# Performance work log

Measured on AMD Instinct MI355X. Metric: run time of the kernel, lower is better.

## Reference

```python
import jax, jax.numpy as jnp
import numpy as np

B, N, C, H = 2, 2048, 1024, 16
D = C // H
SCALE = D ** -0.5


def setup_inputs() -> dict:
    key = jax.random.key(0)
    ks = jax.random.split(key, 5)
    x = jax.random.normal(ks[0], (B, N, C), dtype=jnp.float32)
    # causal mask, broadcast over batch: True = attend
    attention_mask = jnp.broadcast_to(jnp.tril(jnp.ones((N, N), dtype=bool)), (B, N, N))
    w_qkv = jax.random.normal(ks[1], (3 * C, C), dtype=jnp.float32) * (C ** -0.5)
    b_qkv = jax.random.normal(ks[2], (3 * C,), dtype=jnp.float32) * 0.02
    w_proj = jax.random.normal(ks[3], (C, C), dtype=jnp.float32) * (C ** -0.5)
    b_proj = jax.random.normal(ks[4], (C,), dtype=jnp.float32) * 0.02
    return {"x": x, "attention_mask": attention_mask, "w_qkv": w_qkv,
            "b_qkv": b_qkv, "w_proj": w_proj, "b_proj": b_proj}


def reference(x, attention_mask, w_qkv, b_qkv, w_proj, b_proj):
    b, n, c = x.shape
    qkv = x @ w_qkv.T + b_qkv                      # [B,N,3C]
    qkv = qkv.reshape(b, n, 3, H, D).transpose(2, 0, 3, 1, 4)  # [3,B,H,N,D]
    q, k, v = qkv[0], qkv[1], qkv[2]
    dots = jnp.einsum('bhid,bhjd->bhij', q, k) * SCALE
    mask_value = -jnp.finfo(dots.dtype).max
    dots = jnp.where(attention_mask[:, None, :, :], dots, mask_value)
    attn = jax.nn.softmax(dots.astype(jnp.float32), axis=-1).astype(dots.dtype)
    out = jnp.einsum('bhij,bhjd->bhid', attn, v)   # [B,H,N,D]
    # NOTE: original code reshapes WITHOUT transposing heads back - faithful.
    out = out.reshape(b, n, c)
    return out @ w_proj.T + b_proj
```

## Files before the change

kernel.cpp:

```cpp
#include <hip/hip_runtime.h>
#include <hip/hip_bf16.h>
#include <stdint.h>

#define SL_F 0.18033688011112043f

typedef unsigned short u16;
typedef unsigned int u32;
typedef __attribute__((ext_vector_type(8))) short bf16x8;
typedef __attribute__((ext_vector_type(4))) float f32x4;

__device__ __forceinline__ u16 f2bf(float f) {
    union { float f; u32 u; } v; v.f = f;
    return (u16)((v.u + 0x7fffu + ((v.u >> 16) & 1u)) >> 16);
}
__device__ __forceinline__ u32 pack2bf(float a, float b) {
    union { __hip_bfloat162 h; u32 u; } p;
    p.h = __float22bfloat162_rn(make_float2(a, b));
    return p.u;
}

__device__ __forceinline__ void gl_lds16(const u16* g, u16* l) {
    __builtin_amdgcn_global_load_lds(
        (const __attribute__((address_space(1))) u32*)g,
        (__attribute__((address_space(3))) u32*)l, 16, 0, 0);
}

__global__ __launch_bounds__(256) void convert_k(
    const float4* __restrict__ x, const float4* __restrict__ w1,
    const float4* __restrict__ w2,
    ushort4* __restrict__ xb, ushort4* __restrict__ w1b, ushort4* __restrict__ w2b)
{
    const int i = blockIdx.x * 256 + threadIdx.x;
    const int XN = 4096 * 1024 / 4, W1 = 3072 * 1024 / 4;
    float4 v; ushort4* dst;
    if (i < XN)            { v = x[i];            dst = &xb[i]; }
    else if (i < XN + W1)  { v = w1[i - XN];      dst = &w1b[i - XN]; }
    else                   { v = w2[i - XN - W1]; dst = &w2b[i - XN - W1]; }
    ushort4 o;
    o.x = f2bf(v.x); o.y = f2bf(v.y); o.z = f2bf(v.z); o.w = f2bf(v.w);
    *dst = o;
}

template<int NT, int EPI>
__global__ __launch_bounds__(256) void gemm_nt(
    const u16* __restrict__ A, const u16* __restrict__ Bw,
    const float* __restrict__ bias,
    u16* __restrict__ Qb, u16* __restrict__ Kb, u16* __restrict__ VTb,
    float* __restrict__ Out)
{
    constexpr int NBF = NT / 32;
    constexpr int BGRP = NT / 16;
    __shared__ __align__(16) u16 Al[2][8 * 512];
    __shared__ __align__(16) u16 Bl[2][BGRP * 512];
    const int tid = threadIdx.x;
    const int lane = tid & 63;
    const int w = tid >> 6;
    const int la = lane & 15, qd = lane >> 4;
    const int K = 1024;
    const int m0 = blockIdx.y * 128;
    const int n0 = blockIdx.x * NT;
    const int wm = (w >> 1) * 64, wn = (w & 1) * (NT / 2);

    const u16* Ag0 = A + (size_t)(m0 + (2 * w) * 16 + la) * K + qd * 8;
    const u16* Ag1 = A + (size_t)(m0 + (2 * w + 1) * 16 + la) * K + qd * 8;
    const int bg0 = (BGRP == 8) ? 2 * w : w;
    const u16* Bg0 = Bw + (size_t)(n0 + bg0 * 16 + la) * K + qd * 8;
    const u16* Bg1 = Bw + (size_t)(n0 + (2 * w + 1) * 16 + la) * K + qd * 8;

    auto stage = [&](int k0, int b) {
        gl_lds16(Ag0 + k0, &Al[b][(2 * w) * 512]);
        gl_lds16(Ag1 + k0, &Al[b][(2 * w + 1) * 512]);
        gl_lds16(Bg0 + k0, &Bl[b][bg0 * 512]);
        if (BGRP == 8)
            gl_lds16(Bg1 + k0, &Bl[b][(2 * w + 1) * 512]);
    };

    f32x4 acc[4][NBF] = {};
    int buf = 0;
    stage(0, 0);

    for (int k0 = 0; k0 < K; k0 += 32) {
        __syncthreads();
        if (k0 + 32 < K) stage(k0 + 32, buf ^ 1);

        bf16x8 af[4], bfr[NBF];
#pragma unroll
        for (int i = 0; i < 4; i++)
            af[i] = *(const bf16x8*)&Al[buf][(((unsigned)wm >> 4) + i) * 512 + lane * 8];
#pragma unroll
        for (int j = 0; j < NBF; j++)
            bfr[j] = *(const bf16x8*)&Bl[buf][(((unsigned)wn >> 4) + j) * 512 + lane * 8];
#pragma unroll
        for (int i = 0; i < 4; i++)
#pragma unroll
            for (int j = 0; j < NBF; j++)
                acc[i][j] = __builtin_amdgcn_mfma_f32_16x16x32_bf16(
                    af[i], bfr[j], acc[i][j], 0, 0, 0);
        buf ^= 1;
    }

#pragma unroll
    for (int j = 0; j < NBF; j++) {
        const int col = n0 + wn + j * 16 + la;
        const float bv = bias[col];
        if (EPI == 0) {
            const int t = col >> 10, hd = col & 1023, h = hd >> 6, d = hd & 63;
#pragma unroll
            for (int i = 0; i < 4; i++)
#pragma unroll
                for (int r = 0; r < 4; r++) {
                    const int row = m0 + wm + i * 16 + qd * 4 + r;
                    const int b = row >> 11, n = row & 2047;
                    const int bh = b * 16 + h;
                    const u16 val = f2bf(acc[i][j][r] + bv);
                    if (t == 0)      Qb[((size_t)bh * 2048 + n) * 64 + d] = val;
                    else if (t == 1) Kb[((size_t)bh * 2048 + n) * 64 + d] = val;
                    else             VTb[((size_t)bh * 64 + d) * 2048 + n] = val;
                }
        } else {
#pragma unroll
            for (int i = 0; i < 4; i++)
#pragma unroll
                for (int r = 0; r < 4; r++) {
                    const int row = m0 + wm + i * 16 + qd * 4 + r;
                    Out[(size_t)row * 1024 + col] = acc[i][j][r] + bv;
                }
        }
    }
}

__global__ __launch_bounds__(256) void attn_k(
    const u16* __restrict__ Qb, const u16* __restrict__ Kb,
    const u16* __restrict__ VTb, u16* __restrict__ Ob)
{
    __shared__ __align__(16) u16 Kl[2][16 * 512];
    __shared__ __align__(16) u16 Vl[2][16 * 512];
    __shared__ __align__(16) u16 Pl[4][16 * 72];
    const int bh = blockIdx.x & 31;
    const int pair = blockIdx.x >> 5;
    const int tid = threadIdx.x;
    const int lane = tid & 63;
    const int w = tid >> 6;
    const int la = lane & 15, qd = lane >> 4;

    const u16* Kbase = Kb + (size_t)bh * 2048 * 64;
    const u16* Vbase = VTb + (size_t)bh * 64 * 2048;
    u16* Pw = &Pl[w][0];

    u32 ksrc[4], vsrc[4];
#pragma unroll
    for (int t = 0; t < 4; t++) {
        const int ck = 4 * w + t;
        ksrc[t] = (u32)((ck >> 1) * 16 + la) * 64 + (ck & 1) * 32 + qd * 8;
        vsrc[t] = (u32)((ck >> 2) * 16 + la) * 2048 + (ck & 3) * 32 + qd * 8;
    }
    auto stage = [&](int j0, int b) {
#pragma unroll
        for (int t = 0; t < 4; t++) {
            gl_lds16(Kbase + (u32)j0 * 64 + ksrc[t], &Kl[b][(4 * w + t) * 512]);
            gl_lds16(Vbase + (u32)j0 + vsrc[t], &Vl[b][(4 * w + t) * 512]);
        }
    };

    int buf = 0;
    stage(0, 0);

    for (int half = 0; half < 2; half++) {
        const int tile = (half == 0) ? pair : 31 - pair;
        const int q0 = tile * 64 + w * 16;
        const int jmax = (tile >> 1) * 128;
        const int qrow = q0 + la;

        const u16* Qp = Qb + ((size_t)bh * 2048 + q0 + la) * 64 + qd * 8;
        const bf16x8 qf0 = *(const bf16x8*)Qp;
        const bf16x8 qf1 = *(const bf16x8*)(Qp + 32);

        f32x4 o[4] = {};
        float lsum = 0.f;

        for (int j0 = 0; j0 <= jmax; j0 += 128) {
            __syncthreads();

            const int nj = (j0 + 128 <= jmax) ? (j0 + 128) : ((half == 0) ? 0 : -1);
            if (nj >= 0) stage(nj, buf ^ 1);

            f32x4 s[8];
#pragma unroll
            for (int c = 0; c < 8; c++) {
                f32x4 z = {};
                const bf16x8 kf0 = *(const bf16x8*)&Kl[buf][(c * 2 + 0) * 512 + lane * 8];
                const bf16x8 kf1 = *(const bf16x8*)&Kl[buf][(c * 2 + 1) * 512 + lane * 8];
                z = __builtin_amdgcn_mfma_f32_16x16x32_bf16(kf0, qf0, z, 0, 0, 0);
                z = __builtin_amdgcn_mfma_f32_16x16x32_bf16(kf1, qf1, z, 0, 0, 0);
                s[c] = z;
            }

            if (j0 == jmax) {
#pragma unroll
                for (int c = 0; c < 8; c++)
#pragma unroll
                    for (int r = 0; r < 4; r++) {
                        const int j = j0 + c * 16 + qd * 4 + r;
                        float v = s[c][r] * SL_F;
                        v = (j > qrow) ? -1e30f : v;
                        s[c][r] = __builtin_amdgcn_exp2f(v);
                    }
            } else {
#pragma unroll
                for (int c = 0; c < 8; c++)
#pragma unroll
                    for (int r = 0; r < 4; r++)
                        s[c][r] = __builtin_amdgcn_exp2f(s[c][r] * SL_F);
            }
#pragma unroll
            for (int c = 0; c < 8; c++)
#pragma unroll
                for (int r = 0; r < 4; r++)
                    lsum += s[c][r];

#pragma unroll
            for (int hh = 0; hh < 2; hh++) {
#pragma unroll
                for (int c = 0; c < 4; c++) {
                    uint2 pw;
                    pw.x = pack2bf(s[hh * 4 + c][0], s[hh * 4 + c][1]);
                    pw.y = pack2bf(s[hh * 4 + c][2], s[hh * 4 + c][3]);
                    *(uint2*)&Pw[la * 72 + c * 16 + qd * 4] = pw;
                }
                const bf16x8 pf0 = *(const bf16x8*)&Pw[la * 72 + qd * 8];
                const bf16x8 pf1 = *(const bf16x8*)&Pw[la * 72 + 32 + qd * 8];
#pragma unroll
                for (int c2 = 0; c2 < 4; c2++) {
                    const bf16x8 vf0 = *(const bf16x8*)&Vl[buf][(c2 * 4 + hh * 2 + 0) * 512 + lane * 8];
                    const bf16x8 vf1 = *(const bf16x8*)&Vl[buf][(c2 * 4 + hh * 2 + 1) * 512 + lane * 8];
                    o[c2] = __builtin_amdgcn_mfma_f32_16x16x32_bf16(pf0, vf0, o[c2], 0, 0, 0);
                    o[c2] = __builtin_amdgcn_mfma_f32_16x16x32_bf16(pf1, vf1, o[c2], 0, 0, 0);
                }
            }
            buf ^= 1;
        }

        lsum += __shfl_xor(lsum, 16, 64);
        lsum += __shfl_xor(lsum, 32, 64);
        float rinv[4];
#pragma unroll
        for (int r = 0; r < 4; r++)
            rinv[r] = 1.0f / __shfl(lsum, qd * 4 + r, 64);

        u16* Op = Ob + (size_t)bh * 2048 * 64;
#pragma unroll
        for (int c2 = 0; c2 < 4; c2++)
#pragma unroll
            for (int r = 0; r < 4; r++) {
                const int row = q0 + qd * 4 + r;
                Op[(size_t)row * 64 + c2 * 16 + la] = f2bf(o[c2][r] * rinv[r]);
            }
    }
}

extern "C" void kernel_launch(void* const* d_in, const int* in_sizes, int n_in,
                              void* d_out, int out_size, void* d_ws, size_t ws_size,
                              hipStream_t stream)
{
    const float* x     = (const float*)d_in[0];
    const float* wqkv  = (const float*)d_in[2];
    const float* bqkv  = (const float*)d_in[3];
    const float* wproj = (const float*)d_in[4];
    const float* bproj = (const float*)d_in[5];
    float* out = (float*)d_out;

    u16* ws     = (u16*)d_ws;
    u16* xb     = ws;
    u16* wqkvb  = xb + 4096 * 1024;
    u16* wprojb = wqkvb + 3072 * 1024;
    u16* Qb     = wprojb + 1024 * 1024;
    u16* Kb     = Qb + 32 * 2048 * 64;
    u16* VTb    = Kb + 32 * 2048 * 64;
    u16* Ob     = VTb + 32 * 2048 * 64;

    convert_k<<<dim3(8192), dim3(256), 0, stream>>>(
        (const float4*)x, (const float4*)wqkv, (const float4*)wproj,
        (ushort4*)xb, (ushort4*)wqkvb, (ushort4*)wprojb);

    gemm_nt<128, 0><<<dim3(24, 32), dim3(256), 0, stream>>>(
        xb, wqkvb, bqkv, Qb, Kb, VTb, (float*)nullptr);

    attn_k<<<dim3(512), dim3(256), 0, stream>>>(Qb, Kb, VTb, Ob);

    gemm_nt<64, 1><<<dim3(16, 32), dim3(256), 0, stream>>>(
        Ob, wprojb, bproj, (u16*)nullptr, (u16*)nullptr, (u16*)nullptr, out);
}
```

Measured before the change: 228.2 us.

## Warp-specialize GEMMs into producer/consumer waves with 4-stage LDS ring

Replaces the double-buffered GEMM with a warp-specialized design. Two waves issue global-to-LDS loads into a 4-stage ring and two waves run MFMA, synchronizing through LDS atomic counters and spin-waits instead of __syncthreads. The QKV GEMM now uses a 64-wide N tile, so it launches twice as many blocks. The goal is to overlap loads with compute more deeply, at the cost of only two waves doing math per block, spin-loop overhead, and possible visibility hazards between global_load_lds completion and the flag updates.

Result: slower. 254.0 us (+11.3%).

```diff
diff --git a/kernel.cpp b/kernel.cpp
--- a/kernel.cpp
+++ b/kernel.cpp
@@ -24,6 +24,8 @@
         (const __attribute__((address_space(1))) u32*)g,
         (__attribute__((address_space(3))) u32*)l, 16, 0, 0);
 }
+
+#define WAITCNT_VM(n) (((n) & 0xF) | (7u << 4) | (15u << 8) | (((n) >> 4) << 14))
 
 __global__ __launch_bounds__(256) void convert_k(
     const float4* __restrict__ x, const float4* __restrict__ w1,
@@ -41,90 +43,112 @@
     *dst = o;
 }
 
-template<int NT, int EPI>
-__global__ __launch_bounds__(256) void gemm_nt(
+template<int EPI>
+__global__ __launch_bounds__(256) void gemm_pc(
     const u16* __restrict__ A, const u16* __restrict__ Bw,
     const float* __restrict__ bias,
     u16* __restrict__ Qb, u16* __restrict__ Kb, u16* __restrict__ VTb,
     float* __restrict__ Out)
 {
-    constexpr int NBF = NT / 32;
-    constexpr int BGRP = NT / 16;
-    __shared__ __align__(16) u16 Al[2][8 * 512];
-    __shared__ __align__(16) u16 Bl[2][BGRP * 512];
+    __shared__ __align__(16) u16 Asl[4][8 * 512];
+    __shared__ __align__(16) u16 Bsl[4][4 * 512];
+    __shared__ int ready[32];
+    __shared__ int cons[32];
     const int tid = threadIdx.x;
     const int lane = tid & 63;
     const int w = tid >> 6;
     const int la = lane & 15, qd = lane >> 4;
     const int K = 1024;
     const int m0 = blockIdx.y * 128;
-    const int n0 = blockIdx.x * NT;
-    const int wm = (w >> 1) * 64, wn = (w & 1) * (NT / 2);
-
-    const u16* Ag0 = A + (size_t)(m0 + (2 * w) * 16 + la) * K + qd * 8;
-    const u16* Ag1 = A + (size_t)(m0 + (2 * w + 1) * 16 + la) * K + qd * 8;
-    const int bg0 = (BGRP == 8) ? 2 * w : w;
-    const u16* Bg0 = Bw + (size_t)(n0 + bg0 * 16 + la) * K + qd * 8;
-    const u16* Bg1 = Bw + (size_t)(n0 + (2 * w + 1) * 16 + la) * K + qd * 8;
-
-    auto stage = [&](int k0, int b) {
-        gl_lds16(Ag0 + k0, &Al[b][(2 * w) * 512]);
-        gl_lds16(Ag1 + k0, &Al[b][(2 * w + 1) * 512]);
-        gl_lds16(Bg0 + k0, &Bl[b][bg0 * 512]);
-        if (BGRP == 8)
-            gl_lds16(Bg1 + k0, &Bl[b][(2 * w + 1) * 512]);
-    };
-
-    f32x4 acc[4][NBF] = {};
-    int buf = 0;
-    stage(0, 0);
-
-    for (int k0 = 0; k0 < K; k0 += 32) {
-        __syncthreads();
-        if (k0 + 32 < K) stage(k0 + 32, buf ^ 1);
-
-        bf16x8 af[4], bfr[NBF];
-#pragma unroll
-        for (int i = 0; i < 4; i++)
-            af[i] = *(const bf16x8*)&Al[buf][(((unsigned)wm >> 4) + i) * 512 + lane * 8];
-#pragma unroll
-        for (int j = 0; j < NBF; j++)
-            bfr[j] = *(const bf16x8*)&Bl[buf][(((unsigned)wn >> 4) + j) * 512 + lane * 8];
-#pragma unroll
-        for (int i = 0; i < 4; i++)
-#pragma unroll
-            for (int j = 0; j < NBF; j++)
-                acc[i][j] = __builtin_amdgcn_mfma_f32_16x16x32_bf16(
-                    af[i], bfr[j], acc[i][j], 0, 0, 0);
-        buf ^= 1;
-    }
-
-#pragma unroll
-    for (int j = 0; j < NBF; j++) {
-        const int col = n0 + wn + j * 16 + la;
-        const float bv = bias[col];
-        if (EPI == 0) {
-            const int t = col >> 10, hd = col & 1023, h = hd >> 6, d = hd & 63;
+    const int n0 = blockIdx.x * 64;
+
+    if (tid < 32) { ready[tid] = 0; cons[tid] = 0; }
+    __syncthreads();
+
+    if (w >= 2) {
+        const int p = w - 2;
+        const u16* ag[4]; const u16* bg[2];
+#pragma unroll
+        for (int t = 0; t < 4; t++)
+            ag[t] = A + (size_t)(m0 + (4 * p + t) * 16 + la) * K + qd * 8;
+#pragma unroll
+        for (int t = 0; t < 2; t++)
+            bg[t] = Bw + (size_t)(n0 + (2 * p + t) * 16 + la) * K + qd * 8;
+
+        for (int k = 0; k < 32; k++) {
+            if (k >= 4)
+                while (__hip_atomic_load(&cons[k - 4], __ATOMIC_ACQUIRE,
+                                         __HIP_MEMORY_SCOPE_WORKGROUP) < 2) {}
+            const int s = k & 3, k0 = k * 32;
+#pragma unroll
+            for (int t = 0; t < 4; t++)
+                gl_lds16(ag[t] + k0, &Asl[s][(4 * p + t) * 512]);
+#pragma unroll
+            for (int t = 0; t < 2; t++)
+                gl_lds16(bg[t] + k0, &Bsl[s][(2 * p + t) * 512]);
+            if (k >= 1) {
+                __builtin_amdgcn_s_waitcnt(WAITCNT_VM(6));
+                if (lane == 0)
+                    __hip_atomic_fetch_add(&ready[k - 1], 1, __ATOMIC_RELEASE,
+                                           __HIP_MEMORY_SCOPE_WORKGROUP);
+            }
+        }
+        __builtin_amdgcn_s_waitcnt(WAITCNT_VM(0));
+        if (lane == 0)
+            __hip_atomic_fetch_add(&ready[31], 1, __ATOMIC_RELEASE,
+                                   __HIP_MEMORY_SCOPE_WORKGROUP);
+    } else {
+        const int c = w;
+        f32x4 acc[4][4] = {};
+        for (int k = 0; k < 32; k++) {
+            while (__hip_atomic_load(&ready[k], __ATOMIC_ACQUIRE,
+                                     __HIP_MEMORY_SCOPE_WORKGROUP) < 2) {}
+            const int s = k & 3;
+            bf16x8 af[4], bfr[4];
 #pragma unroll
             for (int i = 0; i < 4; i++)
-#pragma unroll
-                for (int r = 0; r < 4; r++) {
-                    const int row = m0 + wm + i * 16 + qd * 4 + r;
-                    const int b = row >> 11, n = row & 2047;
-                    const int bh = b * 16 + h;
-                    const u16 val = f2bf(acc[i][j][r] + bv);
-                    if (t == 0)      Qb[((size_t)bh * 2048 + n) * 64 + d] = val;
-                    else if (t == 1) Kb[((size_t)bh * 2048 + n) * 64 + d] = val;
-                    else             VTb[((size_t)bh * 64 + d) * 2048 + n] = val;
-                }
-        } else {
+                af[i] = *(const bf16x8*)&Asl[s][(4 * c + i) * 512 + lane * 8];
+#pragma unroll
+            for (int j = 0; j < 4; j++)
+                bfr[j] = *(const bf16x8*)&Bsl[s][j * 512 + lane * 8];
 #pragma unroll
             for (int i = 0; i < 4; i++)
 #pragma unroll
-                for (int r = 0; r < 4; r++) {
-                    const int row = m0 + wm + i * 16 + qd * 4 + r;
-                    Out[(size_t)row * 1024 + col] = acc[i][j][r] + bv;
-                }
+                for (int j = 0; j < 4; j++)
+                    acc[i][j] = __builtin_amdgcn_mfma_f32_16x16x32_bf16(
+                        af[i], bfr[j], acc[i][j], 0, 0, 0);
+            if (lane == 0)
+                __hip_atomic_fetch_add(&cons[k], 1, __ATOMIC_RELEASE,
+                                       __HIP_MEMORY_SCOPE_WORKGROUP);
+        }
+
+#pragma unroll
+        for (int j = 0; j < 4; j++) {
+            const int col = n0 + j * 16 + la;
+            const float bv = bias[col];
+            if (EPI == 0) {
+                const int t = col >> 10, hd = col & 1023, h = hd >> 6, d = hd & 63;
+#pragma unroll
+                for (int i = 0; i < 4; i++)
+#pragma unroll
+                    for (int r = 0; r < 4; r++) {
+                        const int row = m0 + c * 64 + i * 16 + qd * 4 + r;
+                        const int b = row >> 11, n = row & 2047;
+                        const int bh = b * 16 + h;
+                        const u16 val = f2bf(acc[i][j][r] + bv);
+                        if (t == 0)      Qb[((size_t)bh * 2048 + n) * 64 + d] = val;
+                        else if (t == 1) Kb[((size_t)bh * 2048 + n) * 64 + d] = val;
+                        else             VTb[((size_t)bh * 64 + d) * 2048 + n] = val;
+                    }
+            } else {
+#pragma unroll
+                for (int i = 0; i < 4; i++)
+#pragma unroll
+                    for (int r = 0; r < 4; r++) {
+                        const int row = m0 + c * 64 + i * 16 + qd * 4 + r;
+                        Out[(size_t)row * 1024 + col] = acc[i][j][r] + bv;
+                    }
+            }
         }
     }
 }
@@ -282,11 +306,11 @@
         (const float4*)x, (const float4*)wqkv, (const float4*)wproj,
         (ushort4*)xb, (ushort4*)wqkvb, (ushort4*)wprojb);
 
-    gemm_nt<128, 0><<<dim3(24, 32), dim3(256), 0, stream>>>(
+    gemm_pc<0><<<dim3(48, 32), dim3(256), 0, stream>>>(
         xb, wqkvb, bqkv, Qb, Kb, VTb, (float*)nullptr);
 
     attn_k<<<dim3(512), dim3(256), 0, stream>>>(Qb, Kb, VTb, Ob);
 
-    gemm_nt<64, 1><<<dim3(16, 32), dim3(256), 0, stream>>>(
+    gemm_pc<1><<<dim3(16, 32), dim3(256), 0, stream>>>(
         Ob, wprojb, bproj, (u16*)nullptr, (u16*)nullptr, (u16*)nullptr, out);
 }
```

## Replace global_load_lds staging with register-prefetched double-buffered GEMM pipeline

Applied to the files above, without the earlier changes.

The GEMM mainloop now loads tiles from global memory into registers two k-steps ahead, then writes them to the alternate LDS buffer after the MFMA block. Each step ends with an explicit lgkmcnt wait plus barrier. This replaces the direct global-to-LDS loads and the __syncthreads at the top of every iteration, with the goal of hiding global latency behind compute. The cost is higher register pressure and extra LDS write instructions.

Measured after the change: 245.6 us. 7.6% more time.

```diff
diff --git a/kernel.cpp b/kernel.cpp
--- a/kernel.cpp
+++ b/kernel.cpp
@@ -23,6 +23,10 @@
     __builtin_amdgcn_global_load_lds(
         (const __attribute__((address_space(1))) u32*)g,
         (__attribute__((address_space(3))) u32*)l, 16, 0, 0);
+}
+
+__device__ __forceinline__ void lds_barrier() {
+    asm volatile("s_waitcnt lgkmcnt(0)\n\ts_barrier" ::: "memory");
 }
 
 __global__ __launch_bounds__(256) void convert_k(
@@ -50,6 +54,7 @@
 {
     constexpr int NBF = NT / 32;
     constexpr int BGRP = NT / 16;
+    constexpr int BPW = BGRP / 4;
     __shared__ __align__(16) u16 Al[2][8 * 512];
     __shared__ __align__(16) u16 Bl[2][BGRP * 512];
     const int tid = threadIdx.x;
@@ -61,42 +66,75 @@
     const int n0 = blockIdx.x * NT;
     const int wm = (w >> 1) * 64, wn = (w & 1) * (NT / 2);
 
-    const u16* Ag0 = A + (size_t)(m0 + (2 * w) * 16 + la) * K + qd * 8;
-    const u16* Ag1 = A + (size_t)(m0 + (2 * w + 1) * 16 + la) * K + qd * 8;
-    const int bg0 = (BGRP == 8) ? 2 * w : w;
-    const u16* Bg0 = Bw + (size_t)(n0 + bg0 * 16 + la) * K + qd * 8;
-    const u16* Bg1 = Bw + (size_t)(n0 + (2 * w + 1) * 16 + la) * K + qd * 8;
-
-    auto stage = [&](int k0, int b) {
-        gl_lds16(Ag0 + k0, &Al[b][(2 * w) * 512]);
-        gl_lds16(Ag1 + k0, &Al[b][(2 * w + 1) * 512]);
-        gl_lds16(Bg0 + k0, &Bl[b][bg0 * 512]);
-        if (BGRP == 8)
-            gl_lds16(Bg1 + k0, &Bl[b][(2 * w + 1) * 512]);
-    };
+    const u16* asrc[2]; const u16* bsrc[BPW];
+#pragma unroll
+    for (int t = 0; t < 2; t++)
+        asrc[t] = A + (size_t)(m0 + (2 * w + t) * 16 + la) * K + qd * 8;
+#pragma unroll
+    for (int t = 0; t < BPW; t++)
+        bsrc[t] = Bw + (size_t)(n0 + (BPW * w + t) * 16 + la) * K + qd * 8;
+
+    bf16x8 a0[2], a1[2], b0[BPW], b1[BPW];
+#pragma unroll
+    for (int t = 0; t < 2; t++)   a0[t] = *(const bf16x8*)(asrc[t]);
+#pragma unroll
+    for (int t = 0; t < BPW; t++) b0[t] = *(const bf16x8*)(bsrc[t]);
+#pragma unroll
+    for (int t = 0; t < 2; t++)   a1[t] = *(const bf16x8*)(asrc[t] + 32);
+#pragma unroll
+    for (int t = 0; t < BPW; t++) b1[t] = *(const bf16x8*)(bsrc[t] + 32);
+
+#pragma unroll
+    for (int t = 0; t < 2; t++)
+        *(bf16x8*)&Al[0][(2 * w + t) * 512 + lane * 8] = a0[t];
+#pragma unroll
+    for (int t = 0; t < BPW; t++)
+        *(bf16x8*)&Bl[0][(BPW * w + t) * 512 + lane * 8] = b0[t];
+    lds_barrier();
 
     f32x4 acc[4][NBF] = {};
-    int buf = 0;
-    stage(0, 0);
-
-    for (int k0 = 0; k0 < K; k0 += 32) {
-        __syncthreads();
-        if (k0 + 32 < K) stage(k0 + 32, buf ^ 1);
-
+
+    auto phase = [&](int k, bf16x8 (&curA)[2], bf16x8 (&curB)[BPW],
+                     bf16x8 (&nxtA)[2], bf16x8 (&nxtB)[BPW]) {
+        const int kb = k & 1;
         bf16x8 af[4], bfr[NBF];
 #pragma unroll
         for (int i = 0; i < 4; i++)
-            af[i] = *(const bf16x8*)&Al[buf][(((unsigned)wm >> 4) + i) * 512 + lane * 8];
+            af[i] = *(const bf16x8*)&Al[kb][(((unsigned)wm >> 4) + i) * 512 + lane * 8];
 #pragma unroll
         for (int j = 0; j < NBF; j++)
-            bfr[j] = *(const bf16x8*)&Bl[buf][(((unsigned)wn >> 4) + j) * 512 + lane * 8];
+            bfr[j] = *(const bf16x8*)&Bl[kb][(((unsigned)wn >> 4) + j) * 512 + lane * 8];
+
+        if (k + 2 < 32) {
+#pragma unroll
+            for (int t = 0; t < 2; t++)
+                nxtA[t] = *(const bf16x8*)(asrc[t] + (k + 2) * 32);
+#pragma unroll
+            for (int t = 0; t < BPW; t++)
+                nxtB[t] = *(const bf16x8*)(bsrc[t] + (k + 2) * 32);
+        }
+
 #pragma unroll
         for (int i = 0; i < 4; i++)
 #pragma unroll
             for (int j = 0; j < NBF; j++)
                 acc[i][j] = __builtin_amdgcn_mfma_f32_16x16x32_bf16(
                     af[i], bfr[j], acc[i][j], 0, 0, 0);
-        buf ^= 1;
+
+        if (k + 1 < 32) {
+#pragma unroll
+            for (int t = 0; t < 2; t++)
+                *(bf16x8*)&Al[kb ^ 1][(2 * w + t) * 512 + lane * 8] = curA[t];
+#pragma unroll
+            for (int t = 0; t < BPW; t++)
+                *(bf16x8*)&Bl[kb ^ 1][(BPW * w + t) * 512 + lane * 8] = curB[t];
+            lds_barrier();
+        }
+    };
+
+    for (int k = 0; k < 32; k += 2) {
+        phase(k,     a1, b1, a0, b0);
+        phase(k + 1, a0, b0, a1, b1);
     }
 
 #pragma unroll
```
